# Kernel tuning notes

Measured on AMD Instinct MI355X. Metric: run time of the kernel, lower is better.

Reference implementation:

```python
import jax, jax.numpy as jnp
import numpy as np

N_NODES = 100000
N_EDGES = 1600000


def setup_inputs() -> dict:
    key = jax.random.key(0)
    ks = jax.random.split(key, 6)
    x = jax.random.normal(ks[0], (N_NODES, 128), dtype=jnp.float32)
    edge_src = jax.random.randint(ks[1], (N_EDGES,), 0, N_NODES, dtype=jnp.int64)
    edge_dst = jax.random.randint(ks[2], (N_EDGES,), 0, N_NODES, dtype=jnp.int64)
    # GCNConv weights (bias=False); glorot-like scaling
    W1 = jax.random.normal(ks[3], (128, 64), dtype=jnp.float32) * (1.0 / np.sqrt(128))
    W2 = jax.random.normal(ks[4], (64, 64), dtype=jnp.float32) * (1.0 / np.sqrt(64))
    W3 = jax.random.normal(ks[5], (64, 40), dtype=jnp.float32) * (1.0 / np.sqrt(64))
    return {"x": x, "edge_src": edge_src, "edge_dst": edge_dst,
            "W1": W1, "W2": W2, "W3": W3}


def reference(x, edge_src, edge_dst, W1, W2, W3):
    # SGC forward (eval mode: dropout is identity).
    # Each GCNConv(normalize=False, bias=False): out = A @ (h @ W)
    n = x.shape[0]

    def conv(h, W):
        hw = h @ W                      # [N, d_out] dense transform
        msgs = hw[edge_src]             # [E, d_out] gather over edges
        return jax.ops.segment_sum(msgs, edge_dst, num_segments=n)  # scatter-add

    h = conv(x, W1)
    h = conv(h, W2)
    h = conv(h, W3)
    return jax.nn.log_softmax(h, axis=-1)
```

## Files before the change

### kernel.cpp

```cpp
#include <hip/hip_runtime.h>
#include <hip/hip_fp16.h>
#include <math.h>


#define BW    128
#define NBMAX 1024
#define BCAP  3072
#define D     40
#define RS    64
#define NPW   12
#define PCHUNK 4096

typedef unsigned short u16;
typedef unsigned int   u32;

static __device__ inline u32 hadd2u(u32 a, u32 b) {
    __half2 ha = *(__half2*)&a, hb = *(__half2*)&b;
    __half2 r = __hadd2(ha, hb);
    return *(u32*)&r;
}

__global__ void k_w12(const float* __restrict__ W1, const float* __restrict__ W2,
                      float* __restrict__ W12, int* __restrict__ gcnt) {
    int idx = blockIdx.x * blockDim.x + threadIdx.x;
    if (blockIdx.x == 0) {
        for (int i = threadIdx.x; i < NBMAX; i += blockDim.x) gcnt[i] = 0;
    }
    if (idx >= 128 * 64) return;
    int r = idx >> 6, c = idx & 63;
    float acc = 0.f;
#pragma unroll
    for (int k = 0; k < 64; ++k) acc += W1[r * 64 + k] * W2[k * 64 + c];
    W12[idx] = acc;
}

__global__ void k_wc(const float* __restrict__ W12, const float* __restrict__ W3,
                     float* __restrict__ Wc) {
    int idx = blockIdx.x * blockDim.x + threadIdx.x;
    if (idx >= 128 * 40) return;
    int r = idx / 40, c = idx - r * 40;
    float acc = 0.f;
#pragma unroll
    for (int k = 0; k < 64; ++k) acc += W12[r * 64 + k] * W3[k * 40 + c];
    Wc[idx] = acc;
}

__global__ void k_gp(const float4* __restrict__ x4, const float4* __restrict__ Wc4,
                     u16* __restrict__ yout, int n_nodes,
                     const int* __restrict__ src, const int* __restrict__ dst,
                     int* __restrict__ gcnt, int* __restrict__ part,
                     int E, int nb, int npart) {
    __shared__ union {
        struct { int h[NBMAX]; int base[NBMAX]; } p;
        float4 wc[1280];
    } sm;
    int t = threadIdx.x;

    if ((int)blockIdx.x < npart) {
        int e0 = blockIdx.x * PCHUNK;
        int e1 = min(e0 + PCHUNK, E);
        for (int i = t; i < nb; i += 256) sm.p.h[i] = 0;
        __syncthreads();
        for (int e = e0 + t; e < e1; e += 1024) {
#pragma unroll
            for (int u = 0; u < 4; ++u) {
                int ee = e + u * 256;
                if (ee < e1) atomicAdd(&sm.p.h[dst[ee] >> 7], 1);
            }
        }
        __syncthreads();
        for (int i = t; i < nb; i += 256) {
            int c = sm.p.h[i];
            sm.p.base[i] = c ? atomicAdd(&gcnt[i], c) : 0;
        }
        __syncthreads();
        for (int i = t; i < nb; i += 256) sm.p.h[i] = 0;
        __syncthreads();
        for (int eb = e0 + t; eb < e1; eb += 2048) {
            int dd[8], ss[8], pp[8];
#pragma unroll
            for (int u = 0; u < 8; ++u) {
                int e = eb + u * 256;
                bool v = e < e1;
                dd[u] = v ? dst[e] : 0;
                ss[u] = v ? src[e] : 0;
            }
#pragma unroll
            for (int u = 0; u < 8; ++u) {
                int e = eb + u * 256;
                int b = dd[u] >> 7;
                pp[u] = (e < e1) ? (sm.p.base[b] + atomicAdd(&sm.p.h[b], 1)) : BCAP;
            }
#pragma unroll
            for (int u = 0; u < 8; ++u) {
                int b = dd[u] >> 7;
                if (pp[u] < BCAP)
                    part[(size_t)b * BCAP + pp[u]] = (ss[u] << 7) | (dd[u] & 127);
            }
        }
    } else {
        for (int i = t; i < 1280; i += 256) sm.wc[i] = Wc4[i];
        __syncthreads();
        int tid = ((int)blockIdx.x - npart) * 256 + t;
        int node = tid / 5, j0 = tid - node * 5;
        if (node >= n_nodes) return;
        float4 a0 = {0.f, 0.f, 0.f, 0.f}, a1 = {0.f, 0.f, 0.f, 0.f};
        const float4* xr = x4 + (size_t)node * 32;
#pragma unroll
        for (int k4 = 0; k4 < 32; ++k4) {
            float4 v = xr[k4];
#pragma unroll
            for (int kk = 0; kk < 4; ++kk) {
                float c = (kk == 0) ? v.x : (kk == 1) ? v.y : (kk == 2) ? v.z : v.w;
                float4 w0 = sm.wc[(k4 * 4 + kk) * 10 + j0 * 2];
                float4 w1 = sm.wc[(k4 * 4 + kk) * 10 + j0 * 2 + 1];
                a0.x += c * w0.x; a0.y += c * w0.y; a0.z += c * w0.z; a0.w += c * w0.w;
                a1.x += c * w1.x; a1.y += c * w1.y; a1.z += c * w1.z; a1.w += c * w1.w;
            }
        }
        __half2 h0 = __floats2half2_rn(a0.x, a0.y);
        __half2 h1 = __floats2half2_rn(a0.z, a0.w);
        __half2 h2 = __floats2half2_rn(a1.x, a1.y);
        __half2 h3 = __floats2half2_rn(a1.z, a1.w);
        uint4 st;
        st.x = *(u32*)&h0; st.y = *(u32*)&h1; st.z = *(u32*)&h2; st.w = *(u32*)&h3;
        *(uint4*)(yout + (size_t)node * RS + j0 * 8) = st;
    }
}

__global__ void k_csr(const int* __restrict__ part, const int* __restrict__ gcnt,
                      int2* __restrict__ offs2, int* __restrict__ ssort, int N) {
    __shared__ int cnt[BW];
    __shared__ int pos[BW];
    __shared__ int cur[BW];
    __shared__ int wsum[2];
    int b = blockIdx.x, t = threadIdx.x;
    int m = min(gcnt[b], BCAP);
    const int* bp = part + (size_t)b * BCAP;
    if (t < BW) cnt[t] = 0;
    __syncthreads();
    for (int k = t; k < m; k += 256)
        atomicAdd(&cnt[bp[k] & 127], 1);
    __syncthreads();
    int v = 0, inc = 0;
    if (t < BW) {
        v = cnt[t];
        inc = v;
#pragma unroll
        for (int off = 1; off < 64; off <<= 1) {
            int u = __shfl_up(inc, off, 64);
            if ((t & 63) >= off) inc += u;
        }
        if ((t & 63) == 63) wsum[t >> 6] = inc;
    }
    __syncthreads();
    int node0 = b * BW;
    if (t < BW) {
        int local = ((t >= 64) ? wsum[0] : 0) + inc - v;
        pos[t] = local;
        cur[t] = 0;
        if (node0 + t < N)
            offs2[node0 + t] = make_int2(b * BCAP + local, b * BCAP + local + v);
    }
    __syncthreads();
    for (int k = t; k < m; k += 256) {
        int p = bp[k];
        int r = p & 127;
        int loc = atomicAdd(&cur[r], 1);
        ssort[(size_t)b * BCAP + pos[r] + loc] = p >> 7;
    }
}

template <int FINAL>
__global__ void k_agg(const u16* __restrict__ yin, void* __restrict__ youtv,
                      const int2* __restrict__ offs2, const int* __restrict__ srcs,
                      int n_nodes) {
    int wid = (blockIdx.x * blockDim.x + threadIdx.x) >> 6;
    int lane = threadIdx.x & 63;
    int g = lane / 5;
    int sub = lane - g * 5;
    int node = wid * NPW + g;
    bool nv = (g < NPW) && (node < n_nodes);
    int2 be = offs2[nv ? node : 0];
    int beg = be.x;
    int deg = nv ? (be.y - be.x) : 0;
    u32 suboff = (u32)sub * 16u;
    u32 c0 = 0, c1 = 0, c2 = 0, c3 = 0;
    for (int k = 0; __any(k < deg); k += 5) {
        int sv = (k + sub < deg) ? srcs[beg + k + sub] : 0;
#pragma unroll
        for (int j = 0; j < 5; ++j) {
            int s = __shfl(sv, g * 5 + j, 64);
            if (k + j < deg) {
                uint4 w = *(const uint4*)((const char*)yin +
                              (size_t)(((u32)s << 7) + suboff));
                c0 = hadd2u(c0, w.x); c1 = hadd2u(c1, w.y);
                c2 = hadd2u(c2, w.z); c3 = hadd2u(c3, w.w);
            }
        }
    }
    if (FINAL) {
        float2 f0 = __half22float2(*(__half2*)&c0);
        float2 f1 = __half22float2(*(__half2*)&c1);
        float2 f2 = __half22float2(*(__half2*)&c2);
        float2 f3 = __half22float2(*(__half2*)&c3);
        int s1 = sub + 1; s1 = (s1 >= 5) ? s1 - 5 : s1;
        int s2 = sub + 2; s2 = (s2 >= 5) ? s2 - 5 : s2;
        int s4 = sub + 4; s4 = (s4 >= 5) ? s4 - 5 : s4;
        int r1 = g * 5 + s1, r2 = g * 5 + s2, r4 = g * 5 + s4;
        float m0 = fmaxf(fmaxf(fmaxf(f0.x, f0.y), fmaxf(f1.x, f1.y)),
                         fmaxf(fmaxf(f2.x, f2.y), fmaxf(f3.x, f3.y)));
        float m = fmaxf(m0, __shfl(m0, r1, 64));
        m = fmaxf(m, __shfl(m, r2, 64));
        m = fmaxf(m, __shfl(m0, r4, 64));
        float e0 = __expf(f0.x - m) + __expf(f0.y - m) + __expf(f1.x - m) +
                   __expf(f1.y - m) + __expf(f2.x - m) + __expf(f2.y - m) +
                   __expf(f3.x - m) + __expf(f3.y - m);
        float sm = e0 + __shfl(e0, r1, 64);
        sm = sm + __shfl(sm, r2, 64);
        sm = sm + __shfl(e0, r4, 64);
        float ls = __logf(sm) + m;
        if (nv) {
            float4 o1 = {f0.x - ls, f0.y - ls, f1.x - ls, f1.y - ls};
            float4 o2 = {f2.x - ls, f2.y - ls, f3.x - ls, f3.y - ls};
            float* op = (float*)youtv + (size_t)node * D + sub * 8;
            *(float4*)op = o1;
            *(float4*)(op + 4) = o2;
        }
    } else {
        if (nv) {
            uint4 st = {c0, c1, c2, c3};
            *(uint4*)((u16*)youtv + (size_t)node * RS + sub * 8) = st;
        }
    }
}

extern "C" void kernel_launch(void* const* d_in, const int* in_sizes, int n_in,
                              void* d_out, int out_size, void* d_ws, size_t ws_size,
                              hipStream_t stream) {
    const float* x   = (const float*)d_in[0];
    const int* esrc  = (const int*)d_in[1];
    const int* edst  = (const int*)d_in[2];
    const float* W1  = (const float*)d_in[3];
    const float* W2  = (const float*)d_in[4];
    const float* W3  = (const float*)d_in[5];
    int N = in_sizes[0] / 128;
    int E = in_sizes[1];
    float* out = (float*)d_out;

    int nb = (N + BW - 1) / BW;

    char* ws = (char*)d_ws;
    auto alloc = [&](size_t bytes) {
        char* p = ws;
        ws += (bytes + 255) & ~(size_t)255;
        return p;
    };
    u16* bufA   = (u16*)alloc((size_t)N * RS * sizeof(u16));
    u16* bufB   = (u16*)alloc((size_t)N * RS * sizeof(u16));
    int* part   = (int*)bufB;
    int* ssort  = (int*)alloc((size_t)nb * BCAP * sizeof(int));
    int2* offs2 = (int2*)alloc((size_t)N * sizeof(int2));
    float* W12  = (float*)alloc(128 * 64 * sizeof(float));
    float* Wc   = (float*)alloc(128 * 40 * sizeof(float));
    int* gcnt   = (int*)alloc(NBMAX * sizeof(int));

    k_w12<<<(128 * 64 + 255) / 256, 256, 0, stream>>>(W1, W2, W12, gcnt);
    k_wc<<<(128 * 40 + 255) / 256, 256, 0, stream>>>(W12, W3, Wc);

    int npart = (E + PCHUNK - 1) / PCHUNK;
    int ngemm = (N * 5 + 255) / 256;
    k_gp<<<npart + ngemm, 256, 0, stream>>>((const float4*)x, (const float4*)Wc,
                                            bufA, N, esrc, edst, gcnt, part,
                                            E, nb, npart);

    k_csr<<<nb, 256, 0, stream>>>(part, gcnt, offs2, ssort, N);

    int nwaves = (N + NPW - 1) / NPW;
    int agg_grid = (nwaves + 3) / 4;
    k_agg<0><<<agg_grid, 256, 0, stream>>>(bufA, bufB, offs2, ssort, N);
    k_agg<0><<<agg_grid, 256, 0, stream>>>(bufB, bufA, offs2, ssort, N);
    k_agg<1><<<agg_grid, 256, 0, stream>>>(bufA, out, offs2, ssort, N);
}
```

Baseline: 174.2 us.

## Split features into per-XCD planes and aggregate one node-plane per thread

Stores the 40-wide fp16 feature matrix as five contiguous 8-column planes instead of 64-stride rows. Each thread now gathers one 16-byte chunk per edge for one node and one plane, with four independent accumulators. Blocks are mapped so each XCD works on a contiguous range of planes, which keeps each plane's gather footprint small enough to stay in that XCD's L2. The log-softmax moves into its own small kernel, and `part` gets a dedicated buffer instead of aliasing bufB. The cost is an extra kernel launch and a per-thread degree loop that can diverge within a wave.

```diff
diff --git a/kernel.cpp b/kernel.cpp
--- a/kernel.cpp
+++ b/kernel.cpp
@@ -7,8 +7,8 @@
 #define NBMAX 1024
 #define BCAP  3072
 #define D     40
-#define RS    64
-#define NPW   12
+#define PLN   5
+#define PSZ   8
 #define PCHUNK 4096
 
 typedef unsigned short u16;
@@ -124,7 +124,7 @@
         __half2 h3 = __floats2half2_rn(a1.z, a1.w);
         uint4 st;
         st.x = *(u32*)&h0; st.y = *(u32*)&h1; st.z = *(u32*)&h2; st.w = *(u32*)&h3;
-        *(uint4*)(yout + (size_t)node * RS + j0 * 8) = st;
+        *(uint4*)(yout + (size_t)j0 * n_nodes * PSZ + (size_t)node * PSZ) = st;
     }
 }
 
@@ -171,67 +171,79 @@
     }
 }
 
-template <int FINAL>
-__global__ void k_agg(const u16* __restrict__ yin, void* __restrict__ youtv,
-                      const int2* __restrict__ offs2, const int* __restrict__ srcs,
-                      int n_nodes) {
-    int wid = (blockIdx.x * blockDim.x + threadIdx.x) >> 6;
-    int lane = threadIdx.x & 63;
-    int g = lane / 5;
-    int sub = lane - g * 5;
-    int node = wid * NPW + g;
-    bool nv = (g < NPW) && (node < n_nodes);
-    int2 be = offs2[nv ? node : 0];
-    int beg = be.x;
-    int deg = nv ? (be.y - be.x) : 0;
-    u32 suboff = (u32)sub * 16u;
+__global__ void k_aggp(const u16* __restrict__ yin, u16* __restrict__ yout,
+                       const int2* __restrict__ offs2, const int* __restrict__ srcs,
+                       int N, int bpx) {
+    int xcd = blockIdx.x & 7, bidx = blockIdx.x >> 3;
+    int w = (xcd * bpx + bidx) * 256 + (int)threadIdx.x;
+    if (w >= PLN * N) return;
+    int plane = w / N;
+    int node = w - plane * N;
+    int2 be = offs2[node];
+    const u16* pb = yin + (size_t)plane * N * PSZ;
+    int k = be.x, end = be.y;
+    u32 a0 = 0, a1 = 0, a2 = 0, a3 = 0;
+    u32 b0 = 0, b1 = 0, b2 = 0, b3 = 0;
     u32 c0 = 0, c1 = 0, c2 = 0, c3 = 0;
-    for (int k = 0; __any(k < deg); k += 5) {
-        int sv = (k + sub < deg) ? srcs[beg + k + sub] : 0;
-#pragma unroll
-        for (int j = 0; j < 5; ++j) {
-            int s = __shfl(sv, g * 5 + j, 64);
-            if (k + j < deg) {
-                uint4 w = *(const uint4*)((const char*)yin +
-                              (size_t)(((u32)s << 7) + suboff));
-                c0 = hadd2u(c0, w.x); c1 = hadd2u(c1, w.y);
-                c2 = hadd2u(c2, w.z); c3 = hadd2u(c3, w.w);
-            }
-        }
-    }
-    if (FINAL) {
-        float2 f0 = __half22float2(*(__half2*)&c0);
-        float2 f1 = __half22float2(*(__half2*)&c1);
-        float2 f2 = __half22float2(*(__half2*)&c2);
-        float2 f3 = __half22float2(*(__half2*)&c3);
-        int s1 = sub + 1; s1 = (s1 >= 5) ? s1 - 5 : s1;
-        int s2 = sub + 2; s2 = (s2 >= 5) ? s2 - 5 : s2;
-        int s4 = sub + 4; s4 = (s4 >= 5) ? s4 - 5 : s4;
-        int r1 = g * 5 + s1, r2 = g * 5 + s2, r4 = g * 5 + s4;
-        float m0 = fmaxf(fmaxf(fmaxf(f0.x, f0.y), fmaxf(f1.x, f1.y)),
-                         fmaxf(fmaxf(f2.x, f2.y), fmaxf(f3.x, f3.y)));
-        float m = fmaxf(m0, __shfl(m0, r1, 64));
-        m = fmaxf(m, __shfl(m, r2, 64));
-        m = fmaxf(m, __shfl(m0, r4, 64));
-        float e0 = __expf(f0.x - m) + __expf(f0.y - m) + __expf(f1.x - m) +
-                   __expf(f1.y - m) + __expf(f2.x - m) + __expf(f2.y - m) +
-                   __expf(f3.x - m) + __expf(f3.y - m);
-        float sm = e0 + __shfl(e0, r1, 64);
-        sm = sm + __shfl(sm, r2, 64);
-        sm = sm + __shfl(e0, r4, 64);
-        float ls = __logf(sm) + m;
-        if (nv) {
-            float4 o1 = {f0.x - ls, f0.y - ls, f1.x - ls, f1.y - ls};
-            float4 o2 = {f2.x - ls, f2.y - ls, f3.x - ls, f3.y - ls};
-            float* op = (float*)youtv + (size_t)node * D + sub * 8;
-            *(float4*)op = o1;
-            *(float4*)(op + 4) = o2;
-        }
-    } else {
-        if (nv) {
-            uint4 st = {c0, c1, c2, c3};
-            *(uint4*)((u16*)youtv + (size_t)node * RS + sub * 8) = st;
-        }
+    u32 d0 = 0, d1 = 0, d2 = 0, d3 = 0;
+    for (; k + 4 <= end; k += 4) {
+        int s0 = srcs[k], s1 = srcs[k + 1], s2 = srcs[k + 2], s3 = srcs[k + 3];
+        uint4 w0 = *(const uint4*)(pb + (size_t)s0 * PSZ);
+        uint4 w1 = *(const uint4*)(pb + (size_t)s1 * PSZ);
+        uint4 w2 = *(const uint4*)(pb + (size_t)s2 * PSZ);
+        uint4 w3 = *(const uint4*)(pb + (size_t)s3 * PSZ);
+        a0 = hadd2u(a0, w0.x); a1 = hadd2u(a1, w0.y);
+        a2 = hadd2u(a2, w0.z); a3 = hadd2u(a3, w0.w);
+        b0 = hadd2u(b0, w1.x); b1 = hadd2u(b1, w1.y);
+        b2 = hadd2u(b2, w1.z); b3 = hadd2u(b3, w1.w);
+        c0 = hadd2u(c0, w2.x); c1 = hadd2u(c1, w2.y);
+        c2 = hadd2u(c2, w2.z); c3 = hadd2u(c3, w2.w);
+        d0 = hadd2u(d0, w3.x); d1 = hadd2u(d1, w3.y);
+        d2 = hadd2u(d2, w3.z); d3 = hadd2u(d3, w3.w);
+    }
+    for (; k < end; ++k) {
+        uint4 w0 = *(const uint4*)(pb + (size_t)srcs[k] * PSZ);
+        a0 = hadd2u(a0, w0.x); a1 = hadd2u(a1, w0.y);
+        a2 = hadd2u(a2, w0.z); a3 = hadd2u(a3, w0.w);
+    }
+    a0 = hadd2u(hadd2u(a0, b0), hadd2u(c0, d0));
+    a1 = hadd2u(hadd2u(a1, b1), hadd2u(c1, d1));
+    a2 = hadd2u(hadd2u(a2, b2), hadd2u(c2, d2));
+    a3 = hadd2u(hadd2u(a3, b3), hadd2u(c3, d3));
+    uint4 st = {a0, a1, a2, a3};
+    *(uint4*)(yout + (size_t)plane * N * PSZ + (size_t)node * PSZ) = st;
+}
+
+__global__ void k_soft(const u16* __restrict__ yin, float* __restrict__ out, int N) {
+    int n = blockIdx.x * blockDim.x + threadIdx.x;
+    if (n >= N) return;
+    float f[40];
+#pragma unroll
+    for (int p = 0; p < PLN; ++p) {
+        uint4 v = *(const uint4*)(yin + (size_t)p * N * PSZ + (size_t)n * PSZ);
+        u32 vv0 = v.x, vv1 = v.y, vv2 = v.z, vv3 = v.w;
+        float2 g0 = __half22float2(*(__half2*)&vv0);
+        float2 g1 = __half22float2(*(__half2*)&vv1);
+        float2 g2 = __half22float2(*(__half2*)&vv2);
+        float2 g3 = __half22float2(*(__half2*)&vv3);
+        f[p * 8 + 0] = g0.x; f[p * 8 + 1] = g0.y;
+        f[p * 8 + 2] = g1.x; f[p * 8 + 3] = g1.y;
+        f[p * 8 + 4] = g2.x; f[p * 8 + 5] = g2.y;
+        f[p * 8 + 6] = g3.x; f[p * 8 + 7] = g3.y;
+    }
+    float m = f[0];
+#pragma unroll
+    for (int i = 1; i < 40; ++i) m = fmaxf(m, f[i]);
+    float s = 0.f;
+#pragma unroll
+    for (int i = 0; i < 40; ++i) s += __expf(f[i] - m);
+    float ls = __logf(s) + m;
+    float4* op = (float4*)(out + (size_t)n * 40);
+#pragma unroll
+    for (int i = 0; i < 10; ++i) {
+        float4 o = {f[i * 4] - ls, f[i * 4 + 1] - ls,
+                    f[i * 4 + 2] - ls, f[i * 4 + 3] - ls};
+        op[i] = o;
     }
 }
 
@@ -256,9 +268,9 @@
         ws += (bytes + 255) & ~(size_t)255;
         return p;
     };
-    u16* bufA   = (u16*)alloc((size_t)N * RS * sizeof(u16));
-    u16* bufB   = (u16*)alloc((size_t)N * RS * sizeof(u16));
-    int* part   = (int*)bufB;
+    u16* bufA   = (u16*)alloc((size_t)N * D * sizeof(u16));
+    u16* bufB   = (u16*)alloc((size_t)N * D * sizeof(u16));
+    int* part   = (int*)alloc((size_t)nb * BCAP * sizeof(int));
     int* ssort  = (int*)alloc((size_t)nb * BCAP * sizeof(int));
     int2* offs2 = (int2*)alloc((size_t)N * sizeof(int2));
     float* W12  = (float*)alloc(128 * 64 * sizeof(float));
@@ -276,9 +288,13 @@
 
     k_csr<<<nb, 256, 0, stream>>>(part, gcnt, offs2, ssort, N);
 
-    int nwaves = (N + NPW - 1) / NPW;
-    int agg_grid = (nwaves + 3) / 4;
-    k_agg<0><<<agg_grid, 256, 0, stream>>>(bufA, bufB, offs2, ssort, N);
-    k_agg<0><<<agg_grid, 256, 0, stream>>>(bufB, bufA, offs2, ssort, N);
-    k_agg<1><<<agg_grid, 256, 0, stream>>>(bufA, out, offs2, ssort, N);
-}
+    int nwork = PLN * N;
+    int nblk = (nwork + 255) / 256;
+    int bpx = (nblk + 7) / 8;
+    int agg_grid = bpx * 8;
+    k_aggp<<<agg_grid, 256, 0, stream>>>(bufA, bufB, offs2, ssort, N, bpx);
+    k_aggp<<<agg_grid, 256, 0, stream>>>(bufB, bufA, offs2, ssort, N, bpx);
+    k_aggp<<<agg_grid, 256, 0, stream>>>(bufA, bufB, offs2, ssort, N, bpx);
+
+    k_soft<<<(N + 255) / 256, 256, 0, stream>>>(bufB, out, N);
+}
```

New measurement: 216.1 us. +24.0%, slower.
